# Optimization experiments

Hardware: AMD Instinct MI355X
Metric: run time of the kernel (lower is better)

Reference implementation:

```python
import jax, jax.numpy as jnp
import numpy as np

D_MODEL = 96
D_INNER = 192        # expand_factor * d_model
D_STATE = 16
DT_RANK = 6          # ceil(d_model / 16)
D_CONV = 4
N_LAYERS = 2
EPS = 1e-5


def conv3d(x, w, b=None, padding=((0, 0), (0, 0), (0, 0)), groups=1):
    # x: (N, C, L, H, W), w: (O, C//groups, kL, kH, kW)
    y = jax.lax.conv_general_dilated(
        x, w, window_strides=(1, 1, 1), padding=padding,
        dimension_numbers=('NCDHW', 'OIDHW', 'NCDHW'),
        feature_group_count=groups)
    return y if b is None else y + b[None, :, None, None, None]


def rmsnorm(x, w):
    # faithful to source: mean of squares over the LAST dim (W)
    return x * jax.lax.rsqrt(jnp.mean(x * x, axis=-1, keepdims=True) + EPS) * w


def mamba_block(x, p):
    # x: (N, d_model, L, H, W)
    L = x.shape[2]
    xz = conv3d(x, p['in_proj_w'], padding=((0, 0), (1, 1), (1, 1)))
    xi, z = xz[:, :D_INNER], xz[:, D_INNER:]
    # causal depthwise temporal conv: pad d_conv-1, crop to L
    xi = conv3d(xi, p['conv1d_w'], p['conv1d_b'],
                padding=((D_CONV - 1, D_CONV - 1), (0, 0), (0, 0)),
                groups=D_INNER)[:, :, :L]
    xi = jax.nn.silu(xi)
    # --- SSM (selective scan, pscan path) ---
    A = -jnp.exp(p['A_log'])                                   # (K, S)
    dbc = conv3d(xi, p['x_proj_w'])                            # (N, dt_rank+2S, L, H, W)
    delta = jax.nn.softplus(conv3d(dbc[:, :DT_RANK], p['dt_proj_w'], p['dt_proj_b']))  # (N, K, L, H, W)
    B = jnp.moveaxis(dbc[:, DT_RANK:DT_RANK + D_STATE], 1, -1)  # (N, L, H, W, S)
    C = dbc[:, DT_RANK + D_STATE:]                              # (N, S, L, H, W)
    deltaA = jnp.exp(delta[..., None] * A[None, :, None, None, None, :])  # (N,K,L,H,W,S)
    BX = delta[..., None] * B[:, None] * xi[..., None]                    # (N,K,L,H,W,S)

    def op(e1, e2):
        a1, b1 = e1
        a2, b2 = e2
        return a1 * a2, a2 * b1 + b2

    _, hs = jax.lax.associative_scan(op, (deltaA, BX), axis=2)  # scan over L
    y = jnp.einsum('nklhws,nslhw->nklhw', hs, C) + p['D'][None, :, None, None, None] * xi
    out = y * jax.nn.silu(z)
    return conv3d(out, p['out_proj_w'])


def _forward(x, in_proj_w, conv1d_w, conv1d_b, x_proj_w, dt_proj_w,
             dt_proj_b, A_log, D, out_proj_w, norm_w):
    for l in range(N_LAYERS):
        p = dict(in_proj_w=in_proj_w[l], conv1d_w=conv1d_w[l], conv1d_b=conv1d_b[l],
                 x_proj_w=x_proj_w[l], dt_proj_w=dt_proj_w[l], dt_proj_b=dt_proj_b[l],
                 A_log=A_log[l], D=D[l], out_proj_w=out_proj_w[l], norm_w=norm_w[l])
        x = mamba_block(rmsnorm(x, p['norm_w']), p) + x   # ResidualBlock
        x = x[:, :, 0:1]                                   # Mamba.forward keeps t=0 only
    return x


def setup_inputs() -> dict:
    key = jax.random.key(0)
    ks = jax.random.split(key, 12)
    Lk = N_LAYERS
    x = jax.random.normal(ks[0], (2, D_MODEL, 8, 24, 24), dtype=jnp.float32)
    in_proj_w = jax.random.normal(ks[1], (Lk, 2 * D_INNER, D_MODEL, 1, 3, 3), jnp.float32) * (D_MODEL * 9) ** -0.5
    conv1d_w = jax.random.normal(ks[2], (Lk, D_INNER, 1, D_CONV, 1, 1), jnp.float32) * D_CONV ** -0.5
    conv1d_b = jax.random.normal(ks[3], (Lk, D_INNER), jnp.float32) * 0.02
    x_proj_w = jax.random.normal(ks[4], (Lk, DT_RANK + 2 * D_STATE, D_INNER, 1, 1, 1), jnp.float32) * D_INNER ** -0.5
    dt_std = DT_RANK ** -0.5
    dt_proj_w = jax.random.uniform(ks[5], (Lk, D_INNER, DT_RANK, 1, 1, 1), jnp.float32, -dt_std, dt_std)
    # dt bias init: inv softplus of dt ~ LogUniform(dt_min, dt_max)
    dt = jnp.exp(jax.random.uniform(ks[6], (Lk, D_INNER), jnp.float32)
                 * (np.log(0.1) - np.log(0.001)) + np.log(0.001))
    dt = jnp.clip(dt, 1e-4, None)
    dt_proj_b = dt + jnp.log(-jnp.expm1(-dt))
    A_log = jnp.log(jnp.tile(jnp.arange(1, D_STATE + 1, dtype=jnp.float32), (Lk, D_INNER, 1)))
    D = jnp.ones((Lk, D_INNER), jnp.float32)
    out_proj_w = jax.random.normal(ks[7], (Lk, D_MODEL, D_INNER, 1, 1, 1), jnp.float32) * D_INNER ** -0.5
    norm_w = jnp.ones((Lk, 1, D_MODEL, 1, 1, 1), jnp.float32)
    return {'x': x, 'in_proj_w': in_proj_w, 'conv1d_w': conv1d_w, 'conv1d_b': conv1d_b,
            'x_proj_w': x_proj_w, 'dt_proj_w': dt_proj_w, 'dt_proj_b': dt_proj_b,
            'A_log': A_log, 'D': D, 'out_proj_w': out_proj_w, 'norm_w': norm_w}


def reference(x, in_proj_w, conv1d_w, conv1d_b, x_proj_w, dt_proj_w,
              dt_proj_b, A_log, D, out_proj_w, norm_w):
    return _forward(x, in_proj_w, conv1d_w, conv1d_b, x_proj_w, dt_proj_w,
                    dt_proj_b, A_log, D, out_proj_w, norm_w)
```

## Files before the change

kernel.cpp:

```cpp
#include <hip/hip_runtime.h>
#include <math.h>

#define NB   2
#define CM   96
#define CI   192
#define CO   384
#define HP   24
#define WP   24
#define PX   576
#define DTR  6
#define NDBC 38
#define CSPLIT 8
#define CCH  12

__device__ __forceinline__ float siluf(float x){ return x / (1.f + expf(-x)); }
__device__ __forceinline__ float softplusf(float x){ return x > 20.f ? x : log1pf(expf(x)); }
__device__ __forceinline__ unsigned short f2bf(float f){
    unsigned u = __float_as_uint(f);
    return (unsigned short)((u + 0x7fffu + ((u >> 16) & 1u)) >> 16);
}
__device__ __forceinline__ float bflo(unsigned u){ return __uint_as_float(u << 16); }
__device__ __forceinline__ float bfhi(unsigned u){ return __uint_as_float(u & 0xffff0000u); }

#define NW_IN (2*CO*CM*9)
#define WQB_L (CM*CO*8)
#define WRB_L (CM*CO)
#define WPT_L (CI*CM)
__global__ void prep_k(const float* __restrict__ ipw, const float* __restrict__ opw,
                       unsigned short* __restrict__ wQb, unsigned short* __restrict__ wRb,
                       float* __restrict__ wpT){
    int idx = blockIdx.x*256 + threadIdx.x;
    if (idx < NW_IN){
        int l = idx / (CO*CM*9);
        int r = idx % (CO*CM*9);
        int o = r / (CM*9);
        int r2 = r % (CM*9);
        int c = r2 / 9;
        int k = r2 % 9;
        unsigned short v = f2bf(ipw[idx]);
        if (k < 8) wQb[(long)l*WQB_L + ((c*CO + o)<<3) + k] = v;
        else       wRb[(long)l*WRB_L + c*CO + o] = v;
    } else {
        int j = idx - NW_IN;
        if (j < 2*CI*CM){
            int l = j / (CI*CM);
            int r = j % (CI*CM);
            int c = r / CM;
            int m = r % CM;
            wpT[l*WPT_L + c*CM + m] = opw[(l*CM + m)*CI + c];
        }
    }
}

__global__ __launch_bounds__(256) void conv_k(
    const float* __restrict__ x, long nStr, long cStr,
    const float* __restrict__ nw,
    const unsigned short* __restrict__ wQb, const unsigned short* __restrict__ wRb,
    float* __restrict__ acc)
{
    __shared__ float hs[CCH][3][28];
    __shared__ float scl[CCH][3];
    int bx  = blockIdx.x;
    int og2 = blockIdx.y;
    int cs  = blockIdx.z;
    int n  = bx / HP, hh = bx % HP;
    int tid = threadIdx.x;
    int c0 = cs*CCH;

    if (tid < CCH*3){
        int c = tid/3, j = tid%3;
        int row = hh + j - 1;
        float s = 0.f;
        if (row >= 0 && row < HP){
            const float4* xp4 = (const float4*)(x + (long)n*nStr + (long)(c0+c)*cStr + row*WP);
            #pragma unroll
            for (int w4 = 0; w4 < WP/4; w4++){
                float4 v = xp4[w4];
                s += v.x*v.x + v.y*v.y + v.z*v.z + v.w*v.w;
            }
            s = rsqrtf(s*(1.0f/WP) + 1e-5f) * nw[c0+c];
        }
        scl[c][j] = s;
    }
    __syncthreads();

    for (int idx = tid; idx < CCH*3*28; idx += 256){
        int c = idx/84; int rem = idx%84; int j = rem/28; int wc = rem%28;
        int row = hh + j - 1;
        float v = 0.f;
        if (row >= 0 && row < HP && wc >= 1 && wc <= WP)
            v = x[(long)n*nStr + (long)(c0+c)*cStr + row*WP + (wc-1)] * scl[c][j];
        hs[c][j][wc] = v;
    }
    __syncthreads();

    int ol = tid & 63;
    int obase = og2*192 + ol;
    int x0 = (tid >> 6) * 6;
    float a0[3][6] = {{0,0,0,0,0,0},{0,0,0,0,0,0},{0,0,0,0,0,0}};
    const uint4* wq4 = (const uint4*)wQb;

    for (int c = 0; c < CCH; c++){
        int cg = c0 + c;
        float r0v[8], r1v[8], r2v[8];
        #pragma unroll
        for (int i = 0; i < 4; i++){
            float2 p0 = *(const float2*)(&hs[c][0][x0] + 2*i);
            float2 p1 = *(const float2*)(&hs[c][1][x0] + 2*i);
            float2 p2 = *(const float2*)(&hs[c][2][x0] + 2*i);
            r0v[2*i] = p0.x; r0v[2*i+1] = p0.y;
            r1v[2*i] = p1.x; r1v[2*i+1] = p1.y;
            r2v[2*i] = p2.x; r2v[2*i+1] = p2.y;
        }
        #pragma unroll
        for (int oc = 0; oc < 3; oc++){
            int o = obase + oc*64;
            uint4 wv = wq4[cg*CO + o];
            float w0 = bflo(wv.x), w1 = bfhi(wv.x);
            float w2 = bflo(wv.y), w3 = bfhi(wv.y);
            float w4 = bflo(wv.z), w5 = bfhi(wv.z);
            float w6 = bflo(wv.w), w7 = bfhi(wv.w);
            float w8 = bflo((unsigned)wRb[cg*CO + o]);
            #pragma unroll
            for (int p = 0; p < 6; p++){
                a0[oc][p] += w0*r0v[p] + w1*r0v[p+1] + w2*r0v[p+2]
                           + w3*r1v[p] + w4*r1v[p+1] + w5*r1v[p+2]
                           + w6*r2v[p] + w7*r2v[p+1] + w8*r2v[p+2];
            }
        }
    }

    #pragma unroll
    for (int oc = 0; oc < 3; oc++){
        float* ap = acc + ((long)(cs*NB + n)*PX + hh*WP + x0)*CO + obase + oc*64;
        #pragma unroll
        for (int p = 0; p < 6; p++) ap[p*CO] = a0[oc][p];
    }
}

__global__ __launch_bounds__(256) void ssmproj_k(
    const float* __restrict__ acc,
    const float* __restrict__ c1w, const float* __restrict__ c1b,
    const float* __restrict__ xpw, const float* __restrict__ dtw,
    const float* __restrict__ dtb, const float* __restrict__ Dp,
    const float* __restrict__ wpT,
    const float* __restrict__ xres, long nStrR, long cStrR,
    float* __restrict__ dst)
{
    __shared__ float gl[4][CI];
    int wave = threadIdx.x >> 6, lane = threadIdx.x & 63;
    int p0 = blockIdx.x*4;
    int p  = p0 + wave;
    int n  = p / PX, px = p % PX;

    float xi[3], sz[3];
    #pragma unroll
    for (int t = 0; t < 3; t++){
        int c = lane + 64*t;
        float xr = 0.f, zr = 0.f;
        #pragma unroll
        for (int q = 0; q < CSPLIT; q++){
            const float* ap = acc + ((long)(q*NB + n)*PX + px)*CO;
            xr += ap[c]; zr += ap[CI + c];
        }
        xi[t] = siluf(xr*c1w[c*4 + 3] + c1b[c]);
        sz[t] = siluf(zr);
    }

    float dbc[NDBC];
    #pragma unroll
    for (int j = 0; j < NDBC; j++){
        float s = 0.f;
        #pragma unroll
        for (int t = 0; t < 3; t++) s += xi[t]*xpw[j*CI + lane + 64*t];
        dbc[j] = s;
    }
    #pragma unroll
    for (int step = 1; step < 64; step <<= 1){
        #pragma unroll
        for (int j = 0; j < NDBC; j++) dbc[j] += __shfl_xor(dbc[j], step, 64);
    }
    float BC = 0.f;
    #pragma unroll
    for (int s = 0; s < 16; s++) BC += dbc[6+s]*dbc[22+s];

    #pragma unroll
    for (int t = 0; t < 3; t++){
        int c = lane + 64*t;
        float dl = dtb[c];
        #pragma unroll
        for (int r = 0; r < DTR; r++) dl += dbc[r]*dtw[c*DTR + r];
        dl = softplusf(dl);
        gl[wave][c] = xi[t]*(dl*BC + Dp[c])*sz[t];
    }
    __syncthreads();

    for (int idx = threadIdx.x; idx < 4*CM; idx += 256){
        int pl = idx / CM, m = idx % CM;
        int pp = p0 + pl;
        int nn = pp / PX, ppx = pp % PX;
        const float* g = gl[pl];
        float s0 = 0.f, s1 = 0.f, s2 = 0.f, s3 = 0.f;
        for (int c = 0; c < CI; c += 4){
            s0 += g[c+0]*wpT[(c+0)*CM + m];
            s1 += g[c+1]*wpT[(c+1)*CM + m];
            s2 += g[c+2]*wpT[(c+2)*CM + m];
            s3 += g[c+3]*wpT[(c+3)*CM + m];
        }
        float s = (s0+s1) + (s2+s3);
        s += xres[(long)nn*nStrR + (long)m*cStrR + ppx];
        dst[(nn*CM + m)*PX + ppx] = s;
    }
}

extern "C" void kernel_launch(void* const* d_in, const int* in_sizes, int n_in,
                              void* d_out, int out_size, void* d_ws, size_t ws_size,
                              hipStream_t stream) {
    const float* x_in = (const float*)d_in[0];
    const float* ipw  = (const float*)d_in[1];
    const float* c1w  = (const float*)d_in[2];
    const float* c1b  = (const float*)d_in[3];
    const float* xpw  = (const float*)d_in[4];
    const float* dtw  = (const float*)d_in[5];
    const float* dtb  = (const float*)d_in[6];
    const float* Dp   = (const float*)d_in[8];
    const float* opw  = (const float*)d_in[9];
    const float* nw   = (const float*)d_in[10];

    char* ws = (char*)d_ws;
    unsigned short* wQb = (unsigned short*)ws;
    unsigned short* wRb = wQb + 2*WQB_L;
    float* wpT = (float*)(wRb + 2*WRB_L);
    float* acc = wpT + 2*WPT_L;
    float* x1  = acc + (long)CSPLIT*NB*PX*CO;

    prep_k<<<(NW_IN + 2*CI*CM + 255)/256, 256, 0, stream>>>(ipw, opw, wQb, wRb, wpT);

    conv_k<<<dim3(NB*HP, 2, CSPLIT), 256, 0, stream>>>(
        x_in, 96L*8*PX, 8L*PX, nw, wQb, wRb, acc);
    ssmproj_k<<<NB*PX/4, 256, 0, stream>>>(
        acc, c1w, c1b, xpw, dtw, dtb, Dp, wpT,
        x_in, 96L*8*PX, 8L*PX, x1);

    conv_k<<<dim3(NB*HP, 2, CSPLIT), 256, 0, stream>>>(
        x1, 96L*PX, (long)PX, nw + CM, wQb + WQB_L, wRb + WRB_L, acc);
    ssmproj_k<<<NB*PX/4, 256, 0, stream>>>(
        acc, c1w + CI*4, c1b + CI, xpw + NDBC*CI, dtw + CI*DTR, dtb + CI, Dp + CI, wpT + WPT_L,
        x1, 96L*PX, (long)PX, (float*)d_out);
}
```

Before: 154.5 us.

## Fuse weight prep into conv kernel via shared-memory bf16 weight staging

Removes the separate prep kernel. Each conv block now loads its 192-output x 12-channel slice of the fp32 in_proj weights, converts it to bf16 and stages it in padded shared memory. The out_proj transpose is folded into the first conv launch, with 48 threads per block each writing one element. This saves a launch and a global round trip for the weights, but every block redoes the conversion and uses about 47KB of shared memory, which may lower occupancy.

```diff
diff --git a/kernel.cpp b/kernel.cpp
--- a/kernel.cpp
+++ b/kernel.cpp
@@ -12,6 +12,8 @@
 #define NDBC 38
 #define CSPLIT 8
 #define CCH  12
+#define IPW_L (CO*CM*9)
+#define WPT_L (CI*CM)
 
 __device__ __forceinline__ float siluf(float x){ return x / (1.f + expf(-x)); }
 __device__ __forceinline__ float softplusf(float x){ return x > 20.f ? x : log1pf(expf(x)); }
@@ -22,42 +24,15 @@
 __device__ __forceinline__ float bflo(unsigned u){ return __uint_as_float(u << 16); }
 __device__ __forceinline__ float bfhi(unsigned u){ return __uint_as_float(u & 0xffff0000u); }
 
-#define NW_IN (2*CO*CM*9)
-#define WQB_L (CM*CO*8)
-#define WRB_L (CM*CO)
-#define WPT_L (CI*CM)
-__global__ void prep_k(const float* __restrict__ ipw, const float* __restrict__ opw,
-                       unsigned short* __restrict__ wQb, unsigned short* __restrict__ wRb,
-                       float* __restrict__ wpT){
-    int idx = blockIdx.x*256 + threadIdx.x;
-    if (idx < NW_IN){
-        int l = idx / (CO*CM*9);
-        int r = idx % (CO*CM*9);
-        int o = r / (CM*9);
-        int r2 = r % (CM*9);
-        int c = r2 / 9;
-        int k = r2 % 9;
-        unsigned short v = f2bf(ipw[idx]);
-        if (k < 8) wQb[(long)l*WQB_L + ((c*CO + o)<<3) + k] = v;
-        else       wRb[(long)l*WRB_L + c*CO + o] = v;
-    } else {
-        int j = idx - NW_IN;
-        if (j < 2*CI*CM){
-            int l = j / (CI*CM);
-            int r = j % (CI*CM);
-            int c = r / CM;
-            int m = r % CM;
-            wpT[l*WPT_L + c*CM + m] = opw[(l*CM + m)*CI + c];
-        }
-    }
-}
-
 __global__ __launch_bounds__(256) void conv_k(
     const float* __restrict__ x, long nStr, long cStr,
     const float* __restrict__ nw,
-    const unsigned short* __restrict__ wQb, const unsigned short* __restrict__ wRb,
-    float* __restrict__ acc)
+    const float* __restrict__ ipw,
+    float* __restrict__ acc,
+    const float* __restrict__ opw,
+    float* __restrict__ wpT)
 {
+    __shared__ unsigned short wu[192*122];
     __shared__ float hs[CCH][3][28];
     __shared__ float scl[CCH][3];
     int bx  = blockIdx.x;
@@ -66,6 +41,14 @@
     int n  = bx / HP, hh = bx % HP;
     int tid = threadIdx.x;
     int c0 = cs*CCH;
+
+    if (opw != nullptr && tid < 48){
+        int lin = bx + (NB*HP)*(og2 + 2*cs);
+        int j = lin*48 + tid;
+        int l = j / WPT_L, r = j % WPT_L;
+        int c = r / CM, m = r % CM;
+        wpT[l*WPT_L + c*CM + m] = opw[(long)(l*CM + m)*CI + c];
+    }
 
     if (tid < CCH*3){
         int c = tid/3, j = tid%3;
@@ -92,16 +75,26 @@
             v = x[(long)n*nStr + (long)(c0+c)*cStr + row*WP + (wc-1)] * scl[c][j];
         hs[c][j][wc] = v;
     }
+
+    {
+        const float* wsrc = ipw + (long)og2*192*(CM*9) + cs*(CCH*9);
+        int o2 = tid / 108, t = tid - o2*108;
+        for (int li = tid; li < 192*108; li += 256){
+            float v = wsrc[(long)o2*(CM*9) + t];
+            wu[o2*122 + (t/9)*10 + (t%9)] = f2bf(v);
+            o2 += 2; t += 40;
+            if (t >= 108){ t -= 108; o2++; }
+        }
+    }
     __syncthreads();
 
     int ol = tid & 63;
     int obase = og2*192 + ol;
     int x0 = (tid >> 6) * 6;
     float a0[3][6] = {{0,0,0,0,0,0},{0,0,0,0,0,0},{0,0,0,0,0,0}};
-    const uint4* wq4 = (const uint4*)wQb;
+    const unsigned* wu32 = (const unsigned*)wu;
 
     for (int c = 0; c < CCH; c++){
-        int cg = c0 + c;
         float r0v[8], r1v[8], r2v[8];
         #pragma unroll
         for (int i = 0; i < 4; i++){
@@ -114,13 +107,14 @@
         }
         #pragma unroll
         for (int oc = 0; oc < 3; oc++){
-            int o = obase + oc*64;
-            uint4 wv = wq4[cg*CO + o];
-            float w0 = bflo(wv.x), w1 = bfhi(wv.x);
-            float w2 = bflo(wv.y), w3 = bfhi(wv.y);
-            float w4 = bflo(wv.z), w5 = bfhi(wv.z);
-            float w6 = bflo(wv.w), w7 = bfhi(wv.w);
-            float w8 = bflo((unsigned)wRb[cg*CO + o]);
+            int wb = (oc*64 + ol)*122 + c*10;
+            unsigned pa = wu32[wb>>1], pb = wu32[(wb>>1)+1];
+            unsigned pc = wu32[(wb>>1)+2], pd = wu32[(wb>>1)+3];
+            float w0 = bflo(pa), w1 = bfhi(pa);
+            float w2 = bflo(pb), w3 = bfhi(pb);
+            float w4 = bflo(pc), w5 = bfhi(pc);
+            float w6 = bflo(pd), w7 = bfhi(pd);
+            float w8 = bflo((unsigned)wu[wb + 8]);
             #pragma unroll
             for (int p = 0; p < 6; p++){
                 a0[oc][p] += w0*r0v[p] + w1*r0v[p+1] + w2*r0v[p+2]
@@ -228,22 +222,18 @@
     const float* nw   = (const float*)d_in[10];
 
     char* ws = (char*)d_ws;
-    unsigned short* wQb = (unsigned short*)ws;
-    unsigned short* wRb = wQb + 2*WQB_L;
-    float* wpT = (float*)(wRb + 2*WRB_L);
+    float* wpT = (float*)ws;
     float* acc = wpT + 2*WPT_L;
     float* x1  = acc + (long)CSPLIT*NB*PX*CO;
 
-    prep_k<<<(NW_IN + 2*CI*CM + 255)/256, 256, 0, stream>>>(ipw, opw, wQb, wRb, wpT);
-
     conv_k<<<dim3(NB*HP, 2, CSPLIT), 256, 0, stream>>>(
-        x_in, 96L*8*PX, 8L*PX, nw, wQb, wRb, acc);
+        x_in, 96L*8*PX, 8L*PX, nw, ipw, acc, opw, wpT);
     ssmproj_k<<<NB*PX/4, 256, 0, stream>>>(
         acc, c1w, c1b, xpw, dtw, dtb, Dp, wpT,
         x_in, 96L*8*PX, 8L*PX, x1);
 
     conv_k<<<dim3(NB*HP, 2, CSPLIT), 256, 0, stream>>>(
-        x1, 96L*PX, (long)PX, nw + CM, wQb + WQB_L, wRb + WRB_L, acc);
+        x1, 96L*PX, (long)PX, nw + CM, ipw + IPW_L, acc, nullptr, nullptr);
     ssmproj_k<<<NB*PX/4, 256, 0, stream>>>(
         acc, c1w + CI*4, c1b + CI, xpw + NDBC*CI, dtw + CI*DTR, dtb + CI, Dp + CI, wpT + WPT_L,
         x1, 96L*PX, (long)PX, (float*)d_out);
```

Result: slower. 189.4 us (+22.6%).
